# Kernel optimization log

Hardware: AMD Instinct MI355X
Metric: run time of the kernel (lower is better)

Reference implementation:

```python
import jax, jax.numpy as jnp
import numpy as np

COMMITMENT_COST = 0.25
ENTROPY_LOSS_RATIO = 0.1
ENTROPY_TEMPERATURE = 0.01


def setup_inputs() -> dict:
    key = jax.random.key(0)
    k1, k2 = jax.random.split(key)
    x = jax.random.normal(k1, (64, 32, 32, 256), dtype=jnp.float32)
    # variance_scaling(fan_in, uniform) init for the codebook parameter
    codebook_size, emb_dim = 1024, 256
    limit = jnp.sqrt(3.0 / emb_dim)
    codebook = jax.random.uniform(k2, (codebook_size, emb_dim), jnp.float32, -limit, limit)
    return {"x": x, "codebook": codebook}


def _squared_euclidean_distance(a, b):
    # a: (n, d), b: (m, d) -> (n, m)
    a2 = jnp.sum(a * a, axis=1, keepdims=True)          # (n, 1)
    b2 = jnp.sum(b * b, axis=1)[None, :]                # (1, m)
    ab = jnp.matmul(a, b.T)                             # (n, m)
    return a2 - 2.0 * ab + b2


def _entropy_loss(affinity, temperature):
    # affinity: (..., K); loss_type='softmax'
    flat = affinity.reshape(-1, affinity.shape[-1]) / temperature
    probs = jax.nn.softmax(flat, axis=-1)
    log_probs = jax.nn.log_softmax(flat + 1e-05, axis=-1)
    target_probs = probs
    avg_probs = jnp.mean(target_probs, axis=0)
    avg_entropy = -jnp.sum(avg_probs * jnp.log(avg_probs + 1e-05))
    sample_entropy = -jnp.mean(jnp.sum(target_probs * log_probs, axis=-1))
    return sample_entropy - avg_entropy


def reference(x, codebook):
    sg = jax.lax.stop_gradient
    emb_dim = x.shape[-1]
    codebook_size = codebook.shape[0]
    flat_x = x.reshape(-1, emb_dim)                              # (N, d)
    distances = _squared_euclidean_distance(flat_x, codebook)    # (N, K)
    distances = distances.reshape(x.shape[:-1] + (codebook_size,))
    encoding_indices = jnp.argmin(distances, axis=-1)            # (B,H,W) int
    # quantize: onehot @ codebook == gather of codebook rows
    quantized = jnp.take(codebook, encoding_indices, axis=0)     # (B,H,W,d)

    e_latent_loss = jnp.mean((sg(quantized) - x) ** 2) * COMMITMENT_COST
    q_latent_loss = jnp.mean((quantized - sg(x)) ** 2)
    entropy_loss = _entropy_loss(-distances, ENTROPY_TEMPERATURE) * ENTROPY_LOSS_RATIO
    loss = (e_latent_loss + q_latent_loss + entropy_loss).astype(jnp.float32)

    # straight-through estimator
    quantized = x + sg(quantized - x)
    return quantized, loss, encoding_indices
```

## Files before the change

### kernel.cpp

```cpp
#include <hip/hip_runtime.h>
#include <math.h>

#define NROWS 65536
#define DIM   256
#define KCB   1024
#define TM    64
#define NBLK  (NROWS / TM)
#define QOFF  (NROWS * DIM)
#define IDXOFF (QOFF + 1)

#define WS_DMIN 0
#define WS_PLP  1
#define WS_AVGP 4
#define WS_C2   (WS_AVGP + 8 * 1024)
#define WS_CBF  (WS_C2 + 1024)

#define DELTA 0.05f
#define XPITCH 260
#define XBU    264

typedef __attribute__((ext_vector_type(8))) __bf16 bf16x8;
typedef __attribute__((ext_vector_type(4))) float  f32x4;
typedef __attribute__((ext_vector_type(8))) unsigned short u16x8;
typedef __attribute__((ext_vector_type(4))) unsigned short u16x4;

#define EP_REDD 0
#define EP_REDK 512
#define EP_RT1  1024
#define EP_RT2  1536
#define EP_GMIN 2048
#define EP_CNT  2112
#define EP_CAND 2176
#define EP_CEX  3200
#define EP_R1F  4224
#define EP_SP   4288
#define EP_KFIN 4352
#define EP_DFIN 4416
#define EP_AVGP 4480
#define EP_SIZE 5504

__device__ __forceinline__ unsigned short f2bf(float f) {
    unsigned u = __float_as_uint(f);
    u += 0x7fffu + ((u >> 16) & 1u);
    return (unsigned short)(u >> 16);
}

__global__ __launch_bounds__(256) void prep_kernel(const float* __restrict__ cb,
                                                   float* __restrict__ ws) {
    int gid = blockIdx.x * 256 + threadIdx.x;
    if (gid < 4) ws[gid] = 0.f;
    if (gid < 8192) ws[WS_AVGP + gid] = 0.f;

    int k  = gid >> 5;
    int s  = gid & 31;
    int kc = s >> 2;
    int qq = s & 3;

    if (gid < 1024) {
        const float4* row = (const float4*)(cb + (size_t)gid * DIM);
        float ssum = 0.f;
#pragma unroll 8
        for (int i = 0; i < DIM / 4; ++i) {
            float4 v = row[i];
            ssum += v.x * v.x + v.y * v.y + v.z * v.z + v.w * v.w;
        }
        ws[WS_C2 + gid] = ssum;
    }

    unsigned short* cbf = (unsigned short*)(ws + WS_CBF);
    const float* src = cb + (size_t)k * DIM + (kc << 5) + (qq << 3);
    float4 v0 = *(const float4*)src, v1 = *(const float4*)(src + 4);
    u16x8 o;
    o[0] = f2bf(v0.x); o[1] = f2bf(v0.y); o[2] = f2bf(v0.z); o[3] = f2bf(v0.w);
    o[4] = f2bf(v1.x); o[5] = f2bf(v1.y); o[6] = f2bf(v1.z); o[7] = f2bf(v1.w);
    *(u16x8*)(cbf + ((((size_t)(kc << 10) + k) << 2) + qq) * 8) = o;
}

__global__ __launch_bounds__(1024, 4) void vq_main(const float* __restrict__ x,
                                                   const float* __restrict__ cb,
                                                   float* __restrict__ ws,
                                                   float* __restrict__ out) {
    __shared__ float epi[EP_SIZE];
    __shared__ float xs[64 * XPITCH];
    __shared__ unsigned short xbf[64 * XBU];

    const int tid  = threadIdx.x;
    const int w    = tid >> 6;
    const int lane = tid & 63;
    const int m    = lane & 15;
    const int q    = lane >> 4;
    const int wc   = w & 7;
    const int rh   = w >> 3;
    const int R0   = blockIdx.x * TM;

    const u16x8* cbf = (const u16x8*)(ws + WS_CBF);
    const u16x8* bbase = cbf + (((wc << 6) + m) << 2) + q;

    u16x8 breg[2][4];
    bf16x8 ah[2];

    float4 t0 = *((const float4*)(x + (size_t)(R0 + (w << 2) + 0) * DIM) + lane);
    float4 t1 = *((const float4*)(x + (size_t)(R0 + (w << 2) + 1) * DIM) + lane);
    float4 t2 = *((const float4*)(x + (size_t)(R0 + (w << 2) + 2) * DIM) + lane);
    float4 t3 = *((const float4*)(x + (size_t)(R0 + (w << 2) + 3) * DIM) + lane);

    {
        const u16x8* p = bbase;
        breg[0][0] = p[0]; breg[0][1] = p[64]; breg[0][2] = p[128]; breg[0][3] = p[192];
    }

    *((float4*)(xs + ((w << 2) + 0) * XPITCH) + lane) = t0;
    *((float4*)(xs + ((w << 2) + 1) * XPITCH) + lane) = t1;
    *((float4*)(xs + ((w << 2) + 2) * XPITCH) + lane) = t2;
    *((float4*)(xs + ((w << 2) + 3) * XPITCH) + lane) = t3;
    {
        u16x4 o;
        o[0] = f2bf(t0.x); o[1] = f2bf(t0.y); o[2] = f2bf(t0.z); o[3] = f2bf(t0.w);
        *(u16x4*)(xbf + ((w << 2) + 0) * XBU + (lane << 2)) = o;
        o[0] = f2bf(t1.x); o[1] = f2bf(t1.y); o[2] = f2bf(t1.z); o[3] = f2bf(t1.w);
        *(u16x4*)(xbf + ((w << 2) + 1) * XBU + (lane << 2)) = o;
        o[0] = f2bf(t2.x); o[1] = f2bf(t2.y); o[2] = f2bf(t2.z); o[3] = f2bf(t2.w);
        *(u16x4*)(xbf + ((w << 2) + 2) * XBU + (lane << 2)) = o;
        o[0] = f2bf(t3.x); o[1] = f2bf(t3.y); o[2] = f2bf(t3.z); o[3] = f2bf(t3.w);
        *(u16x4*)(xbf + ((w << 2) + 3) * XBU + (lane << 2)) = o;
    }

    f32x4 acc[2][8];
#pragma unroll
    for (int a = 0; a < 2; ++a)
#pragma unroll
        for (int b = 0; b < 8; ++b) acc[a][b] = (f32x4)0.f;

    __syncthreads();

    const int rbase = rh << 5;
    ah[0] = __builtin_bit_cast(bf16x8, *(const u16x8*)(xbf + (rbase + m) * XBU + (q << 3)));
    ah[1] = __builtin_bit_cast(bf16x8, *(const u16x8*)(xbf + (rbase + 16 + m) * XBU + (q << 3)));

#pragma unroll
    for (int sub = 0; sub < 16; ++sub) {
        const int pb = sub & 1;
        if (sub < 15) {
            const int ns = sub + 1;
            const u16x8* p = bbase + ((ns >> 1) << 12) + ((ns & 1) << 11);
            breg[pb ^ 1][0] = p[0];   breg[pb ^ 1][1] = p[64];
            breg[pb ^ 1][2] = p[128]; breg[pb ^ 1][3] = p[192];
        }
#pragma unroll
        for (int ct = 0; ct < 4; ++ct) {
            bf16x8 bh = __builtin_bit_cast(bf16x8, breg[pb][ct]);
            int cg = ((sub & 1) << 2) + ct;
            acc[0][cg] = __builtin_amdgcn_mfma_f32_16x16x32_bf16(ah[0], bh, acc[0][cg], 0, 0, 0);
            acc[1][cg] = __builtin_amdgcn_mfma_f32_16x16x32_bf16(ah[1], bh, acc[1][cg], 0, 0, 0);
        }
        if ((sub & 1) == 1 && sub < 15) {
            const int nkc = (sub >> 1) + 1;
            ah[0] = __builtin_bit_cast(bf16x8,
                *(const u16x8*)(xbf + (rbase + m) * XBU + (nkc << 5) + (q << 3)));
            ah[1] = __builtin_bit_cast(bf16x8,
                *(const u16x8*)(xbf + (rbase + 16 + m) * XBU + (nkc << 5) + (q << 3)));
        }
    }

    if (tid < 64) ((int*)(epi + EP_CNT))[tid] = 0;
    epi[EP_AVGP + tid] = 0.f;

    float c2v[8];
#pragma unroll
    for (int cg = 0; cg < 8; ++cg) {
        int col = ((cg >> 2) << 9) + (wc << 6) + ((cg & 3) << 4) + m;
        c2v[cg] = ws[WS_C2 + col];
    }
#pragma unroll
    for (int rt = 0; rt < 2; ++rt) {
#pragma unroll
        for (int reg = 0; reg < 4; ++reg) {
            int row = rbase + (rt << 4) + (q << 2) + reg;
            float md = 3.0e38f; int mk = 0;
#pragma unroll
            for (int cg = 0; cg < 8; ++cg) {
                float g = c2v[cg] - 2.0f * acc[rt][cg][reg];
                acc[rt][cg][reg] = g;
                int col = ((cg >> 2) << 9) + (wc << 6) + ((cg & 3) << 4) + m;
                if (g < md) { md = g; mk = col; }
            }
#pragma unroll
            for (int off = 1; off <= 8; off <<= 1) {
                float od = __shfl_xor(md, off, 64);
                int   ok = __shfl_xor(mk, off, 64);
                if (od < md || (od == md && ok < mk)) { md = od; mk = ok; }
            }
            if (m == 0) {
                epi[EP_REDD + (wc << 6) + row] = md;
                ((int*)(epi + EP_REDK))[(wc << 6) + row] = mk;
            }
        }
    }
    __syncthreads();

    if (tid < 64) {
        float gm = 3.0e38f;
#pragma unroll
        for (int g = 0; g < 8; ++g) {
            float d = epi[EP_REDD + (g << 6) + tid];
            if (d < gm) gm = d;
        }
        epi[EP_GMIN + tid] = gm;
    }
    __syncthreads();

    {
        int* cnt  = (int*)(epi + EP_CNT);
        int* cand = (int*)(epi + EP_CAND);
#pragma unroll
        for (int rt = 0; rt < 2; ++rt) {
#pragma unroll
            for (int reg = 0; reg < 4; ++reg) {
                int row = rbase + (rt << 4) + (q << 2) + reg;
                float gm = epi[EP_GMIN + row];
                float t1 = 0.f, t2 = 0.f;
#pragma unroll
                for (int cg = 0; cg < 8; ++cg) {
                    float g = acc[rt][cg][reg];
                    if (g < gm + DELTA) {
                        int col = ((cg >> 2) << 9) + (wc << 6) + ((cg & 3) << 4) + m;
                        int pos = atomicAdd(&cnt[row], 1);
                        if (pos < 16) cand[(row << 4) + pos] = col;
                    }
                    float z = -100.0f * (g - gm);
                    float e = __expf(z);
                    acc[rt][cg][reg] = e;
                    t1 += e;
                    t2 += e * z;
                }
#pragma unroll
                for (int off = 1; off <= 8; off <<= 1) {
                    t1 += __shfl_xor(t1, off, 64);
                    t2 += __shfl_xor(t2, off, 64);
                }
                if (m == 0) {
                    epi[EP_RT1 + (wc << 6) + row] = t1;
                    epi[EP_RT2 + (wc << 6) + row] = t2;
                }
            }
        }
    }
    __syncthreads();

    if (tid < 64) {
        float T1 = 0.f, T2 = 0.f;
#pragma unroll
        for (int g = 0; g < 8; ++g) {
            T1 += epi[EP_RT1 + (g << 6) + tid];
            T2 += epi[EP_RT2 + (g << 6) + tid];
        }
        float r1 = 1.0f / T1;
        epi[EP_R1F + tid] = r1;
        epi[EP_SP + tid]  = T2 * r1 - logf(T1);
    }
    __syncthreads();

    float sv[8];
    {
        float r1v[2][4];
#pragma unroll
        for (int rt = 0; rt < 2; ++rt)
#pragma unroll
            for (int reg = 0; reg < 4; ++reg)
                r1v[rt][reg] = epi[EP_R1F + rbase + (rt << 4) + (q << 2) + reg];
#pragma unroll
        for (int cg = 0; cg < 8; ++cg) {
            float s = 0.f;
#pragma unroll
            for (int rt = 0; rt < 2; ++rt)
#pragma unroll
                for (int reg = 0; reg < 4; ++reg)
                    s += acc[rt][cg][reg] * r1v[rt][reg];
            s += __shfl_xor(s, 16, 64);
            s += __shfl_xor(s, 32, 64);
            sv[cg] = s;
        }
        if (rh == 0 && lane < 16) {
#pragma unroll
            for (int cg = 0; cg < 8; ++cg) {
                int col = ((cg >> 2) << 9) + (wc << 6) + ((cg & 3) << 4) + m;
                epi[EP_AVGP + col] += sv[cg];
            }
        }
    }
    {
        int* cnt  = (int*)(epi + EP_CNT);
        int* cand = (int*)(epi + EP_CAND);
        int r = tid >> 4;
        int i = tid & 15;
        int n = cnt[r]; if (n > 16) n = 16;
        if (i < n) {
            int k = cand[(r << 4) + i];
            const float4* ax = (const float4*)(xs + r * XPITCH);
            const float4* bx = (const float4*)(cb + (((size_t)k) << 8));
            float ab = 0.f, x2 = 0.f;
#pragma unroll 8
            for (int d4 = 0; d4 < 64; ++d4) {
                float4 a = ax[d4], b = bx[d4];
                ab = fmaf(a.x, b.x, ab);
                ab = fmaf(a.y, b.y, ab);
                ab = fmaf(a.z, b.z, ab);
                ab = fmaf(a.w, b.w, ab);
                x2 += a.x * a.x + a.y * a.y + a.z * a.z + a.w * a.w;
            }
            float t = 2.0f * ab;
            epi[EP_CEX + (r << 4) + i] = (x2 - t) + ws[WS_C2 + k];
        }
    }
    __syncthreads();

    if (rh == 1 && lane < 16) {
#pragma unroll
        for (int cg = 0; cg < 8; ++cg) {
            int col = ((cg >> 2) << 9) + (wc << 6) + ((cg & 3) << 4) + m;
            epi[EP_AVGP + col] += sv[cg];
        }
    }

    if (tid < 64) {
        int* cnt  = (int*)(epi + EP_CNT);
        int* cand = (int*)(epi + EP_CAND);
        int n = cnt[tid]; if (n > 16) n = 16;
        float bd = epi[EP_CEX + (tid << 4)];
        int   bk = cand[(tid << 4)];
        for (int i = 1; i < n; ++i) {
            float d = epi[EP_CEX + (tid << 4) + i];
            int   k = cand[(tid << 4) + i];
            if (d < bd || (d == bd && k < bk)) { bd = d; bk = k; }
        }
        ((int*)(epi + EP_KFIN))[tid] = bk;
        epi[EP_DFIN + tid] = bd;
        out[IDXOFF + R0 + tid] = (float)bk;
    }
    __syncthreads();

#pragma unroll
    for (int rr = 0; rr < 4; ++rr) {
        int r = (w << 2) + rr;
        int k = ((int*)(epi + EP_KFIN))[r];
        f32x4 v = *((const f32x4*)(cb + (((size_t)k) << 8)) + lane);
        __builtin_nontemporal_store(v, (f32x4*)(out + (((size_t)(R0 + r)) << 8)) + lane);
    }
    atomicAdd(ws + WS_AVGP + ((blockIdx.x & 7) << 10) + tid, epi[EP_AVGP + tid]);
    if (tid < 64) {
        float sp = epi[EP_SP + tid];
        float dd = epi[EP_DFIN + tid];
#pragma unroll
        for (int off = 1; off <= 32; off <<= 1) {
            sp += __shfl_xor(sp, off, 64);
            dd += __shfl_xor(dd, off, 64);
        }
        if (tid == 0) {
            atomicAdd(ws + WS_PLP, sp);
            atomicAdd(ws + WS_DMIN, dd);
        }
    }
}

__global__ __launch_bounds__(256) void vq_finalize(const float* __restrict__ ws,
                                                   float* __restrict__ out) {
    __shared__ float red[4];
    int tid = threadIdx.x;
    float part = 0.f;
    for (int k = tid; k < 1024; k += 256) {
        float s = 0.f;
#pragma unroll
        for (int r = 0; r < 8; ++r) s += ws[WS_AVGP + (r << 10) + k];
        float ap = s * (1.0f / 65536.0f);
        part += ap * logf(ap + 1e-5f);
    }
#pragma unroll
    for (int off = 32; off; off >>= 1) part += __shfl_xor(part, off, 64);
    if ((tid & 63) == 0) red[tid >> 6] = part;
    __syncthreads();
    if (tid == 0) {
        float sum_aplog      = red[0] + red[1] + red[2] + red[3];
        float avg_entropy    = -sum_aplog;
        float sample_entropy = -ws[WS_PLP] * (1.0f / 65536.0f);
        float entropy_loss   = (sample_entropy - avg_entropy) * 0.1f;
        float eq = 1.25f * ws[WS_DMIN] * (1.0f / ((float)NROWS * (float)DIM));
        out[QOFF] = eq + entropy_loss;
    }
}

extern "C" void kernel_launch(void* const* d_in, const int* in_sizes, int n_in,
                              void* d_out, int out_size, void* d_ws, size_t ws_size,
                              hipStream_t stream) {
    const float* x  = (const float*)d_in[0];
    const float* cb = (const float*)d_in[1];
    float* out = (float*)d_out;
    float* ws  = (float*)d_ws;

    prep_kernel<<<128, 256, 0, stream>>>(cb, ws);
    vq_main<<<NBLK, 1024, 0, stream>>>(x, cb, ws, out);
    vq_finalize<<<1, 256, 0, stream>>>(ws, out);
}
```

Baseline: 264.7 us.

## Stage codebook tiles through LDS with direct global-to-LDS loads

```diff
diff --git a/kernel.cpp b/kernel.cpp
--- a/kernel.cpp
+++ b/kernel.cpp
@@ -17,12 +17,10 @@
 
 #define DELTA 0.05f
 #define XPITCH 260
-#define XBU    264
 
 typedef __attribute__((ext_vector_type(8))) __bf16 bf16x8;
 typedef __attribute__((ext_vector_type(4))) float  f32x4;
 typedef __attribute__((ext_vector_type(8))) unsigned short u16x8;
-typedef __attribute__((ext_vector_type(4))) unsigned short u16x4;
 
 #define EP_REDD 0
 #define EP_REDK 512
@@ -45,6 +43,20 @@
     return (unsigned short)(u >> 16);
 }
 
+__device__ __forceinline__ bf16x8 cvt8(const float* src) {
+    float4 v0 = *(const float4*)src, v1 = *(const float4*)(src + 4);
+    u16x8 o;
+    o[0] = f2bf(v0.x); o[1] = f2bf(v0.y); o[2] = f2bf(v0.z); o[3] = f2bf(v0.w);
+    o[4] = f2bf(v1.x); o[5] = f2bf(v1.y); o[6] = f2bf(v1.z); o[7] = f2bf(v1.w);
+    return __builtin_bit_cast(bf16x8, o);
+}
+
+__device__ __forceinline__ void gload_lds16(const void* g, void* l) {
+    __builtin_amdgcn_global_load_lds(
+        (const __attribute__((address_space(1))) unsigned int*)g,
+        (__attribute__((address_space(3))) unsigned int*)l, 16, 0, 0);
+}
+
 __global__ __launch_bounds__(256) void prep_kernel(const float* __restrict__ cb,
                                                    float* __restrict__ ws) {
     int gid = blockIdx.x * 256 + threadIdx.x;
@@ -82,7 +94,7 @@
                                                    float* __restrict__ out) {
     __shared__ float epi[EP_SIZE];
     __shared__ float xs[64 * XPITCH];
-    __shared__ unsigned short xbf[64 * XBU];
+    __shared__ u16x8 ldsB[2][2048];
 
     const int tid  = threadIdx.x;
     const int w    = tid >> 6;
@@ -93,10 +105,9 @@
     const int rh   = w >> 3;
     const int R0   = blockIdx.x * TM;
 
-    const u16x8* cbf = (const u16x8*)(ws + WS_CBF);
-    const u16x8* bbase = cbf + (((wc << 6) + m) << 2) + q;
-
-    u16x8 breg[2][4];
+    const char* gB = (const char*)(ws + WS_CBF);
+    const int fragoff = (wc << 8) + (m << 2) + q;
+
     bf16x8 ah[2];
 
     float4 t0 = *((const float4*)(x + (size_t)(R0 + (w << 2) + 0) * DIM) + lane);
@@ -105,25 +116,16 @@
     float4 t3 = *((const float4*)(x + (size_t)(R0 + (w << 2) + 3) * DIM) + lane);
 
     {
-        const u16x8* p = bbase;
-        breg[0][0] = p[0]; breg[0][1] = p[64]; breg[0][2] = p[128]; breg[0][3] = p[192];
+        const char* g = gB + (size_t)tid * 16;
+        char* l = (char*)&ldsB[0][0] + (w << 10);
+        gload_lds16(g, l);
+        gload_lds16(g + 16384, l + 16384);
     }
 
     *((float4*)(xs + ((w << 2) + 0) * XPITCH) + lane) = t0;
     *((float4*)(xs + ((w << 2) + 1) * XPITCH) + lane) = t1;
     *((float4*)(xs + ((w << 2) + 2) * XPITCH) + lane) = t2;
     *((float4*)(xs + ((w << 2) + 3) * XPITCH) + lane) = t3;
-    {
-        u16x4 o;
-        o[0] = f2bf(t0.x); o[1] = f2bf(t0.y); o[2] = f2bf(t0.z); o[3] = f2bf(t0.w);
-        *(u16x4*)(xbf + ((w << 2) + 0) * XBU + (lane << 2)) = o;
-        o[0] = f2bf(t1.x); o[1] = f2bf(t1.y); o[2] = f2bf(t1.z); o[3] = f2bf(t1.w);
-        *(u16x4*)(xbf + ((w << 2) + 1) * XBU + (lane << 2)) = o;
-        o[0] = f2bf(t2.x); o[1] = f2bf(t2.y); o[2] = f2bf(t2.z); o[3] = f2bf(t2.w);
-        *(u16x4*)(xbf + ((w << 2) + 2) * XBU + (lane << 2)) = o;
-        o[0] = f2bf(t3.x); o[1] = f2bf(t3.y); o[2] = f2bf(t3.z); o[3] = f2bf(t3.w);
-        *(u16x4*)(xbf + ((w << 2) + 3) * XBU + (lane << 2)) = o;
-    }
 
     f32x4 acc[2][8];
 #pragma unroll
@@ -134,32 +136,34 @@
     __syncthreads();
 
     const int rbase = rh << 5;
-    ah[0] = __builtin_bit_cast(bf16x8, *(const u16x8*)(xbf + (rbase + m) * XBU + (q << 3)));
-    ah[1] = __builtin_bit_cast(bf16x8, *(const u16x8*)(xbf + (rbase + 16 + m) * XBU + (q << 3)));
+    ah[0] = cvt8(xs + (rbase + m) * XPITCH + (q << 3));
+    ah[1] = cvt8(xs + (rbase + 16 + m) * XPITCH + (q << 3));
 
 #pragma unroll
     for (int sub = 0; sub < 16; ++sub) {
-        const int pb = sub & 1;
+        const int cur = sub & 1;
         if (sub < 15) {
-            const int ns = sub + 1;
-            const u16x8* p = bbase + ((ns >> 1) << 12) + ((ns & 1) << 11);
-            breg[pb ^ 1][0] = p[0];   breg[pb ^ 1][1] = p[64];
-            breg[pb ^ 1][2] = p[128]; breg[pb ^ 1][3] = p[192];
-        }
+            const char* g = gB + (size_t)(sub + 1) * 32768 + (size_t)tid * 16;
+            char* l = (char*)&ldsB[cur ^ 1][0] + (w << 10);
+            gload_lds16(g, l);
+            gload_lds16(g + 16384, l + 16384);
+        }
+        const u16x8* lbc = &ldsB[cur][fragoff];
+        u16x8 f0 = lbc[0], f1 = lbc[64], f2 = lbc[128], f3 = lbc[192];
 #pragma unroll
         for (int ct = 0; ct < 4; ++ct) {
-            bf16x8 bh = __builtin_bit_cast(bf16x8, breg[pb][ct]);
+            u16x8 fr = (ct == 0) ? f0 : (ct == 1) ? f1 : (ct == 2) ? f2 : f3;
+            bf16x8 bh = __builtin_bit_cast(bf16x8, fr);
             int cg = ((sub & 1) << 2) + ct;
             acc[0][cg] = __builtin_amdgcn_mfma_f32_16x16x32_bf16(ah[0], bh, acc[0][cg], 0, 0, 0);
             acc[1][cg] = __builtin_amdgcn_mfma_f32_16x16x32_bf16(ah[1], bh, acc[1][cg], 0, 0, 0);
         }
         if ((sub & 1) == 1 && sub < 15) {
             const int nkc = (sub >> 1) + 1;
-            ah[0] = __builtin_bit_cast(bf16x8,
-                *(const u16x8*)(xbf + (rbase + m) * XBU + (nkc << 5) + (q << 3)));
-            ah[1] = __builtin_bit_cast(bf16x8,
-                *(const u16x8*)(xbf + (rbase + 16 + m) * XBU + (nkc << 5) + (q << 3)));
-        }
+            ah[0] = cvt8(xs + (rbase + m) * XPITCH + (nkc << 5) + (q << 3));
+            ah[1] = cvt8(xs + (rbase + 16 + m) * XPITCH + (nkc << 5) + (q << 3));
+        }
+        if (sub < 15) __syncthreads();
     }
 
     if (tid < 64) ((int*)(epi + EP_CNT))[tid] = 0;
```

After: 248.8 us. -6.0%, faster.

## Stage bf16 codebook tiles through LDS with async global-to-LDS triple buffering

Applied to the files above, without the earlier changes.

```diff
diff --git a/kernel.cpp b/kernel.cpp
--- a/kernel.cpp
+++ b/kernel.cpp
@@ -16,8 +16,7 @@
 #define WS_CBF  (WS_C2 + 1024)
 
 #define DELTA 0.05f
-#define XPITCH 260
-#define XBU    264
+#define XBU   264
 
 typedef __attribute__((ext_vector_type(8))) __bf16 bf16x8;
 typedef __attribute__((ext_vector_type(4))) float  f32x4;
@@ -45,6 +44,12 @@
     return (unsigned short)(u >> 16);
 }
 
+__device__ __forceinline__ void gload_lds16(const void* g, void* l) {
+    __builtin_amdgcn_global_load_lds(
+        (const __attribute__((address_space(1))) unsigned int*)g,
+        (__attribute__((address_space(3))) unsigned int*)l, 16, 0, 0);
+}
+
 __global__ __launch_bounds__(256) void prep_kernel(const float* __restrict__ cb,
                                                    float* __restrict__ ws) {
     int gid = blockIdx.x * 256 + threadIdx.x;
@@ -67,13 +72,20 @@
         ws[WS_C2 + gid] = ssum;
     }
 
+    int h  = k >> 9;
+    int wc = (k >> 6) & 7;
+    int ct = (k >> 4) & 3;
+    int m  = k & 15;
+    int sub = (kc << 1) + h;
+    size_t chunk = ((size_t)sub << 11) + (wc << 8) + (ct << 6) + (qq << 4) + m;
+
     unsigned short* cbf = (unsigned short*)(ws + WS_CBF);
     const float* src = cb + (size_t)k * DIM + (kc << 5) + (qq << 3);
     float4 v0 = *(const float4*)src, v1 = *(const float4*)(src + 4);
     u16x8 o;
     o[0] = f2bf(v0.x); o[1] = f2bf(v0.y); o[2] = f2bf(v0.z); o[3] = f2bf(v0.w);
     o[4] = f2bf(v1.x); o[5] = f2bf(v1.y); o[6] = f2bf(v1.z); o[7] = f2bf(v1.w);
-    *(u16x8*)(cbf + ((((size_t)(kc << 10) + k) << 2) + qq) * 8) = o;
+    *(u16x8*)(cbf + chunk * 8) = o;
 }
 
 __global__ __launch_bounds__(1024, 4) void vq_main(const float* __restrict__ x,
@@ -81,8 +93,8 @@
                                                    float* __restrict__ ws,
                                                    float* __restrict__ out) {
     __shared__ float epi[EP_SIZE];
-    __shared__ float xs[64 * XPITCH];
     __shared__ unsigned short xbf[64 * XBU];
+    __shared__ u16x8 ldsB[3][2048];
 
     const int tid  = threadIdx.x;
     const int w    = tid >> 6;
@@ -93,10 +105,9 @@
     const int rh   = w >> 3;
     const int R0   = blockIdx.x * TM;
 
-    const u16x8* cbf = (const u16x8*)(ws + WS_CBF);
-    const u16x8* bbase = cbf + (((wc << 6) + m) << 2) + q;
-
-    u16x8 breg[2][4];
+    const char* gB = (const char*)(ws + WS_CBF);
+    const int fragoff = (wc << 8) + lane;
+
     bf16x8 ah[2];
 
     float4 t0 = *((const float4*)(x + (size_t)(R0 + (w << 2) + 0) * DIM) + lane);
@@ -105,14 +116,16 @@
     float4 t3 = *((const float4*)(x + (size_t)(R0 + (w << 2) + 3) * DIM) + lane);
 
     {
-        const u16x8* p = bbase;
-        breg[0][0] = p[0]; breg[0][1] = p[64]; breg[0][2] = p[128]; breg[0][3] = p[192];
-    }
-
-    *((float4*)(xs + ((w << 2) + 0) * XPITCH) + lane) = t0;
-    *((float4*)(xs + ((w << 2) + 1) * XPITCH) + lane) = t1;
-    *((float4*)(xs + ((w << 2) + 2) * XPITCH) + lane) = t2;
-    *((float4*)(xs + ((w << 2) + 3) * XPITCH) + lane) = t3;
+        const char* g0 = gB + (size_t)tid * 16;
+        char* l0 = (char*)&ldsB[0][0] + (w << 10);
+        gload_lds16(g0, l0);
+        gload_lds16(g0 + 16384, l0 + 16384);
+        const char* g1 = gB + 32768 + (size_t)tid * 16;
+        char* l1 = (char*)&ldsB[1][0] + (w << 10);
+        gload_lds16(g1, l1);
+        gload_lds16(g1 + 16384, l1 + 16384);
+    }
+
     {
         u16x4 o;
         o[0] = f2bf(t0.x); o[1] = f2bf(t0.y); o[2] = f2bf(t0.z); o[3] = f2bf(t0.w);
@@ -139,26 +152,41 @@
 
 #pragma unroll
     for (int sub = 0; sub < 16; ++sub) {
-        const int pb = sub & 1;
-        if (sub < 15) {
-            const int ns = sub + 1;
-            const u16x8* p = bbase + ((ns >> 1) << 12) + ((ns & 1) << 11);
-            breg[pb ^ 1][0] = p[0];   breg[pb ^ 1][1] = p[64];
-            breg[pb ^ 1][2] = p[128]; breg[pb ^ 1][3] = p[192];
-        }
+        if (sub + 2 <= 15) {
+            const char* g = gB + (size_t)(sub + 2) * 32768 + (size_t)tid * 16;
+            char* l = (char*)&ldsB[(sub + 2) % 3][0] + (w << 10);
+            gload_lds16(g, l);
+            gload_lds16(g + 16384, l + 16384);
+        }
+        const u16x8* lbc = &ldsB[sub % 3][fragoff];
+        u16x8 f0 = lbc[0], f1 = lbc[64], f2 = lbc[128], f3 = lbc[192];
+        __builtin_amdgcn_s_setprio(1);
 #pragma unroll
         for (int ct = 0; ct < 4; ++ct) {
-            bf16x8 bh = __builtin_bit_cast(bf16x8, breg[pb][ct]);
+            u16x8 fr = (ct == 0) ? f0 : (ct == 1) ? f1 : (ct == 2) ? f2 : f3;
+            bf16x8 bh = __builtin_bit_cast(bf16x8, fr);
             int cg = ((sub & 1) << 2) + ct;
             acc[0][cg] = __builtin_amdgcn_mfma_f32_16x16x32_bf16(ah[0], bh, acc[0][cg], 0, 0, 0);
             acc[1][cg] = __builtin_amdgcn_mfma_f32_16x16x32_bf16(ah[1], bh, acc[1][cg], 0, 0, 0);
         }
+        __builtin_amdgcn_s_setprio(0);
         if ((sub & 1) == 1 && sub < 15) {
             const int nkc = (sub >> 1) + 1;
             ah[0] = __builtin_bit_cast(bf16x8,
                 *(const u16x8*)(xbf + (rbase + m) * XBU + (nkc << 5) + (q << 3)));
             ah[1] = __builtin_bit_cast(bf16x8,
                 *(const u16x8*)(xbf + (rbase + 16 + m) * XBU + (nkc << 5) + (q << 3)));
+        }
+        if (sub < 15) {
+            __builtin_amdgcn_sched_barrier(0);
+            if (sub < 14) {
+                asm volatile("s_waitcnt vmcnt(2)" ::: "memory");
+            } else {
+                asm volatile("s_waitcnt vmcnt(0)" ::: "memory");
+            }
+            __builtin_amdgcn_sched_barrier(0);
+            __builtin_amdgcn_s_barrier();
+            __builtin_amdgcn_sched_barrier(0);
         }
     }
 
@@ -296,7 +324,7 @@
         int n = cnt[r]; if (n > 16) n = 16;
         if (i < n) {
             int k = cand[(r << 4) + i];
-            const float4* ax = (const float4*)(xs + r * XPITCH);
+            const float4* ax = (const float4*)(x  + (((size_t)(R0 + r)) << 8));
             const float4* bx = (const float4*)(cb + (((size_t)k) << 8));
             float ab = 0.f, x2 = 0.f;
 #pragma unroll 8
```

New measurement: 271.1 us. +2.4%, slower.
